# Kernel optimization log

Hardware: AMD Instinct MI355X
Metric: run time of the kernel (lower is better)

Reference implementation:

```python
import jax, jax.numpy as jnp
import numpy as np

N_LEVELS = 16
N_FEATURES = 2
RES_BASE = 16.0
RES_FINE = 512.0
LOG2_HASHMAP = 19
HASHMAP_SIZE = 1 << LOG2_HASHMAP
ROOM_MIN = np.zeros(3, np.float32)
ROOM_MAX = np.ones(3, np.float32)
# primes as uint32; low 19 bits of (corner * prime) match int64 math since
# low-k bits of a product depend only on low-k bits of the operands, and the
# final XOR is bitwise followed by mod 2**19 (a power of two -> bit mask).
PRIMES = np.array([1, 2654435761, 805459861], dtype=np.uint32)
# 8 trilinear corners in the same (dx,dy,dz) enumeration as the torch code
OFFSETS = np.array([[dx, dy, dz] for dx in (0, 1) for dy in (0, 1) for dz in (0, 1)], dtype=np.uint32)
OFFSETS_F = OFFSETS.astype(np.float32)


def setup_inputs() -> dict:
    key = jax.random.key(0)
    k1, k2 = jax.random.split(key)
    x = jax.random.uniform(k1, (1048576, 3), dtype=jnp.float32)  # points in unit cube
    embeddings = jax.random.uniform(k2, (HASHMAP_SIZE, N_FEATURES), dtype=jnp.float32,
                                    minval=-1e-4, maxval=1e-4)
    return {"x": x, "embeddings": embeddings}


def reference(x, embeddings):
    # growth factor b = exp((log(res_fine) - log(res_base)) / (L - 1))
    b = jnp.exp((jnp.log(jnp.float32(RES_FINE)) - jnp.log(jnp.float32(RES_BASE))) / (N_LEVELS - 1))
    x_norm = (x - ROOM_MIN) / (ROOM_MAX - ROOM_MIN)  # [N,3]
    feats = []
    for i in range(N_LEVELS):  # fixed small loop over levels
        res = jnp.floor(RES_BASE * b ** i)
        xs = x_norm * res                      # [N,3]
        xi = jnp.floor(xs)                     # [N,3]
        w = xs - xi                            # [N,3] trilinear weights
        corner = xi.astype(jnp.uint32)[:, None, :] + OFFSETS[None]  # [N,8,3]
        h = ((corner[..., 0] * PRIMES[0]) ^ (corner[..., 1] * PRIMES[1])
             ^ (corner[..., 2] * PRIMES[2])) & jnp.uint32(HASHMAP_SIZE - 1)  # [N,8]
        emb = embeddings[h]                    # [N,8,F] gather
        # corner weight = prod_d (off ? w : 1-w)
        cw = jnp.prod(OFFSETS_F[None] * w[:, None, :] + (1.0 - OFFSETS_F[None]) * (1.0 - w[:, None, :]), axis=-1)  # [N,8]
        feats.append(jnp.einsum('nc,ncf->nf', cw, emb))  # [N,F]
    return jnp.concatenate(feats, axis=-1)  # [N, L*F]
```

## Files before the change

### kernel.cpp

```cpp
#include <hip/hip_runtime.h>


#define TBL   (1u << 19)
#define MASK  (TBL - 1u)
#define P2    2654435761u
#define P3    805459861u
#define NBIN  4096
#define CAP   512
#define OVFCAP 65536

typedef _Float16 f16;
typedef f16 f16x2 __attribute__((ext_vector_type(2)));
typedef unsigned long long u64;

static __device__ __constant__ float c_res[16] = {
    16.f, 20.f, 25.f, 32.f, 40.f, 50.f, 64.f, 80.f,
    101.f, 128.f, 161.f, 203.f, 256.f, 322.f, 406.f, 512.f
};

__global__ __launch_bounds__(256) void k_prep(
    const float2* __restrict__ emb, f16x2* __restrict__ tbl,
    unsigned* __restrict__ cnt)
{
    int i = blockIdx.x * 256 + threadIdx.x;
    float2 v = emb[i];
    f16x2 h; h.x = (f16)v.x; h.y = (f16)v.y;
    tbl[i] = h;
    if (i <= NBIN) cnt[i] = 0u;
}

__global__ __launch_bounds__(256) void k_scatter(
    const float* __restrict__ x, unsigned* __restrict__ cnt,
    u64* __restrict__ rec, unsigned* __restrict__ ovf, int np)
{
    int p = blockIdx.x * 256 + threadIdx.x;
    if (p >= np) return;
    float px = x[3 * p + 0], py = x[3 * p + 1], pz = x[3 * p + 2];
    int cx = min(15, (int)(px * 16.0f));
    int cy = min(15, (int)(py * 16.0f));
    int cz = min(15, (int)(pz * 16.0f));
    unsigned key = (unsigned)((cx << 8) | (cy << 4) | cz);
    float fx = px * 16.0f - (float)cx;
    float fy = py * 16.0f - (float)cy;
    float fz = pz * 16.0f - (float)cz;
    unsigned qx = min(32767u, (unsigned)(fmaxf(fx, 0.0f) * 32768.0f));
    unsigned qy = min(32767u, (unsigned)(fmaxf(fy, 0.0f) * 32768.0f));
    unsigned qz = min(16383u, (unsigned)(fmaxf(fz, 0.0f) * 16384.0f));
    u64 r = ((u64)qx << 49) | ((u64)qy << 34) | ((u64)qz << 20) | (unsigned)p;

    unsigned slot = atomicAdd(&cnt[key], 1u);
    if (slot < CAP) {
        rec[(size_t)key * CAP + slot] = r;
    } else {
        unsigned o = atomicAdd(&cnt[NBIN], 1u);
        if (o < OVFCAP) ovf[o] = (unsigned)p;
    }
}

__device__ __forceinline__ void level_global(
    int l, float px, float py, float pz, const f16x2* __restrict__ t,
    float* o0, float* o1)
{
    float res = c_res[l];
    float sx = px * res, sy = py * res, sz = pz * res;
    float fx = floorf(sx), fy = floorf(sy), fz = floorf(sz);
    float wx1 = sx - fx, wy1 = sy - fy, wz1 = sz - fz;
    float wx0 = 1.0f - wx1, wy0 = 1.0f - wy1, wz0 = 1.0f - wz1;

    unsigned ux = (unsigned)fx, uy = (unsigned)fy, uz = (unsigned)fz;
    unsigned hx0 = ux, hx1 = ux + 1u;
    unsigned hy0 = uy * P2, hy1 = (uy + 1u) * P2;
    unsigned hz0 = uz * P3, hz1 = (uz + 1u) * P3;

    f16x2 e000 = t[(hx0 ^ hy0 ^ hz0) & MASK];
    f16x2 e001 = t[(hx0 ^ hy0 ^ hz1) & MASK];
    f16x2 e010 = t[(hx0 ^ hy1 ^ hz0) & MASK];
    f16x2 e011 = t[(hx0 ^ hy1 ^ hz1) & MASK];
    f16x2 e100 = t[(hx1 ^ hy0 ^ hz0) & MASK];
    f16x2 e101 = t[(hx1 ^ hy0 ^ hz1) & MASK];
    f16x2 e110 = t[(hx1 ^ hy1 ^ hz0) & MASK];
    f16x2 e111 = t[(hx1 ^ hy1 ^ hz1) & MASK];

    float wxy00 = wx0 * wy0, wxy01 = wx0 * wy1;
    float wxy10 = wx1 * wy0, wxy11 = wx1 * wy1;
    float c000 = wxy00 * wz0, c001 = wxy00 * wz1;
    float c010 = wxy01 * wz0, c011 = wxy01 * wz1;
    float c100 = wxy10 * wz0, c101 = wxy10 * wz1;
    float c110 = wxy11 * wz0, c111 = wxy11 * wz1;

    float f0 = c000 * (float)e000.x;
    float f1 = c000 * (float)e000.y;
    f0 = fmaf(c001, (float)e001.x, f0);  f1 = fmaf(c001, (float)e001.y, f1);
    f0 = fmaf(c010, (float)e010.x, f0);  f1 = fmaf(c010, (float)e010.y, f1);
    f0 = fmaf(c011, (float)e011.x, f0);  f1 = fmaf(c011, (float)e011.y, f1);
    f0 = fmaf(c100, (float)e100.x, f0);  f1 = fmaf(c100, (float)e100.y, f1);
    f0 = fmaf(c101, (float)e101.x, f0);  f1 = fmaf(c101, (float)e101.y, f1);
    f0 = fmaf(c110, (float)e110.x, f0);  f1 = fmaf(c110, (float)e110.y, f1);
    f0 = fmaf(c111, (float)e111.x, f0);  f1 = fmaf(c111, (float)e111.y, f1);
    *o0 = f0; *o1 = f1;
}

__device__ __forceinline__ unsigned fine_key(u64 r) {
    return ((((unsigned)(r >> 61)) & 7u) << 6) |
           ((((unsigned)(r >> 46)) & 7u) << 3) |
            (((unsigned)(r >> 31)) & 7u);
}

__global__ __launch_bounds__(256) void k_main(
    const u64* __restrict__ rec, const unsigned* __restrict__ cnt,
    const unsigned* __restrict__ ovf,
    const float* __restrict__ x, const f16x2* __restrict__ tbl,
    float* __restrict__ out, int np)
{
    int b = (int)(((blockIdx.x & 7u) << 9) | (blockIdx.x >> 3));
    int tid = threadIdx.x;
    float fbx = (float)(b >> 8), fby = (float)((b >> 4) & 15), fbz = (float)(b & 15);

    __shared__ u64 srec[CAP];
    __shared__ u64 ssort[CAP];
    __shared__ unsigned hist[512];
    __shared__ unsigned scn[256];
    __shared__ float sbuf[256 * 8];

    int n = min((int)cnt[b], CAP);

    for (int i = tid; i < n; i += 256) srec[i] = rec[(size_t)b * CAP + i];
    hist[tid] = 0u; hist[tid + 256] = 0u;
    __syncthreads();
    for (int i = tid; i < n; i += 256) atomicAdd(&hist[fine_key(srec[i])], 1u);
    __syncthreads();
    unsigned a0 = hist[2 * tid], a1 = hist[2 * tid + 1];
    unsigned s = a0 + a1;
    scn[tid] = s;
    __syncthreads();
    for (int d = 1; d < 256; d <<= 1) {
        unsigned v = (tid >= d) ? scn[tid - d] : 0u;
        __syncthreads();
        scn[tid] += v;
        __syncthreads();
    }
    unsigned excl = scn[tid] - s;
    hist[2 * tid] = excl;
    hist[2 * tid + 1] = excl + a0;
    __syncthreads();
    for (int i = tid; i < n; i += 256) {
        u64 r = srec[i];
        unsigned pos = atomicAdd(&hist[fine_key(r)], 1u);
        ssort[pos] = r;
    }
    __syncthreads();

    for (int i0 = 0; i0 < n; i0 += 256) {
        int nb = min(256, n - i0);
        bool act = tid < nb;
        u64 r = ssort[i0 + (act ? tid : 0)];
        unsigned qx = ((unsigned)(r >> 49)) & 32767u;
        unsigned qy = ((unsigned)(r >> 34)) & 32767u;
        unsigned qz = ((unsigned)(r >> 20)) & 16383u;
        float px = (fbx + ((float)qx + 0.5f) * (1.0f / 32768.0f)) * 0.0625f;
        float py = (fby + ((float)qy + 0.5f) * (1.0f / 32768.0f)) * 0.0625f;
        float pz = (fbz + ((float)qz + 0.5f) * (1.0f / 16384.0f)) * 0.0625f;

        #pragma unroll
        for (int g = 0; g < 4; ++g) {
            float fo[8];
            #pragma unroll
            for (int sl = 0; sl < 4; ++sl)
                level_global(4 * g + sl, px, py, pz, tbl, &fo[2 * sl], &fo[2 * sl + 1]);
            *(float4*)&sbuf[tid * 8 + 0] = *(float4*)&fo[0];
            *(float4*)&sbuf[tid * 8 + 4] = *(float4*)&fo[4];
            __syncthreads();
            for (int j = tid; j < 2 * nb; j += 256) {
                int pt = j >> 1, h = j & 1;
                unsigned pj = (unsigned)(ssort[i0 + pt] & 0xFFFFFu);
                float4 v = *(float4*)&sbuf[pt * 8 + h * 4];
                *(float4*)(out + (size_t)pj * 32 + g * 8 + h * 4) = v;
            }
            __syncthreads();
        }
    }

    unsigned oc = min(cnt[NBIN], (unsigned)OVFCAP);
    for (unsigned t = blockIdx.x * 256u + (unsigned)tid; t < oc; t += NBIN * 256u) {
        unsigned p = ovf[t];
        float px = x[3 * p + 0], py = x[3 * p + 1], pz = x[3 * p + 2];
        float* op = out + (size_t)p * 32;
        #pragma unroll
        for (int g = 0; g < 4; ++g) {
            float fo[8];
            #pragma unroll
            for (int sl = 0; sl < 4; ++sl)
                level_global(4 * g + sl, px, py, pz, tbl, &fo[2 * sl], &fo[2 * sl + 1]);
            ((float4*)op)[2 * g + 0] = *(float4*)&fo[0];
            ((float4*)op)[2 * g + 1] = *(float4*)&fo[4];
        }
    }
}

__global__ __launch_bounds__(256) void hashgrid_fwd(
    const float* __restrict__ x, const float* __restrict__ emb,
    float* __restrict__ out, int npts)
{
    int tid = blockIdx.x * 256 + threadIdx.x;
    int p = tid >> 4;
    int l = tid & 15;
    if (p >= npts) return;
    float px = x[p * 3], py = x[p * 3 + 1], pz = x[p * 3 + 2];
    float res = c_res[l];
    float sx = px * res, sy = py * res, sz = pz * res;
    float fx = floorf(sx), fy = floorf(sy), fz = floorf(sz);
    float wx1 = sx - fx, wy1 = sy - fy, wz1 = sz - fz;
    float wx0 = 1.0f - wx1, wy0 = 1.0f - wy1, wz0 = 1.0f - wz1;
    unsigned ux = (unsigned)fx, uy = (unsigned)fy, uz = (unsigned)fz;
    unsigned hx0 = ux, hx1 = ux + 1u;
    unsigned hy0 = uy * P2, hy1 = (uy + 1u) * P2;
    unsigned hz0 = uz * P3, hz1 = (uz + 1u) * P3;
    const float2* e = (const float2*)emb;
    float2 e000 = e[(hx0 ^ hy0 ^ hz0) & MASK];
    float2 e001 = e[(hx0 ^ hy0 ^ hz1) & MASK];
    float2 e010 = e[(hx0 ^ hy1 ^ hz0) & MASK];
    float2 e011 = e[(hx0 ^ hy1 ^ hz1) & MASK];
    float2 e100 = e[(hx1 ^ hy0 ^ hz0) & MASK];
    float2 e101 = e[(hx1 ^ hy0 ^ hz1) & MASK];
    float2 e110 = e[(hx1 ^ hy1 ^ hz0) & MASK];
    float2 e111 = e[(hx1 ^ hy1 ^ hz1) & MASK];
    float wxy00 = wx0 * wy0, wxy01 = wx0 * wy1;
    float wxy10 = wx1 * wy0, wxy11 = wx1 * wy1;
    float c000 = wxy00 * wz0, c001 = wxy00 * wz1;
    float c010 = wxy01 * wz0, c011 = wxy01 * wz1;
    float c100 = wxy10 * wz0, c101 = wxy10 * wz1;
    float c110 = wxy11 * wz0, c111 = wxy11 * wz1;
    float f0 = c000 * e000.x;
    float f1 = c000 * e000.y;
    f0 = fmaf(c001, e001.x, f0);  f1 = fmaf(c001, e001.y, f1);
    f0 = fmaf(c010, e010.x, f0);  f1 = fmaf(c010, e010.y, f1);
    f0 = fmaf(c011, e011.x, f0);  f1 = fmaf(c011, e011.y, f1);
    f0 = fmaf(c100, e100.x, f0);  f1 = fmaf(c100, e100.y, f1);
    f0 = fmaf(c101, e101.x, f0);  f1 = fmaf(c101, e101.y, f1);
    f0 = fmaf(c110, e110.x, f0);  f1 = fmaf(c110, e110.y, f1);
    f0 = fmaf(c111, e111.x, f0);  f1 = fmaf(c111, e111.y, f1);
    float2 o; o.x = f0; o.y = f1;
    ((float2*)out)[p * 16 + l] = o;
}

extern "C" void kernel_launch(void* const* d_in, const int* in_sizes, int n_in,
                              void* d_out, int out_size, void* d_ws, size_t ws_size,
                              hipStream_t stream) {
    const float* x   = (const float*)d_in[0];
    const float* emb = (const float*)d_in[1];
    float* out = (float*)d_out;
    int np = in_sizes[0] / 3;

    size_t szrec = (size_t)NBIN * CAP * 8;
    size_t sztbl = (size_t)TBL * 4;
    size_t szovf = (size_t)OVFCAP * 4;
    size_t szcnt = (size_t)(NBIN + 16) * 4;
    size_t need = szrec + sztbl + szovf + szcnt;

    if (ws_size >= need) {
        char* w = (char*)d_ws;
        u64*      rec = (u64*)(w);
        f16x2*    tbl = (f16x2*)(w + szrec);
        unsigned* ovf = (unsigned*)(w + szrec + sztbl);
        unsigned* cnt = (unsigned*)(w + szrec + sztbl + szovf);

        int pb = (np + 255) / 256;
        k_prep   <<<TBL / 256, 256, 0, stream>>>((const float2*)emb, tbl, cnt);
        k_scatter<<<pb, 256, 0, stream>>>(x, cnt, rec, ovf, np);
        k_main   <<<NBIN, 256, 0, stream>>>(rec, cnt, ovf, x, tbl, out, np);
    } else {
        int total = np * 16;
        hashgrid_fwd<<<(total + 255) / 256, 256, 0, stream>>>(x, emb, out, np);
    }
}
```

Before: 410.1 us.

## Split levels across threads: eight threads per point, two levels each

The main loop now assigns each point to eight threads, each computing two hash-grid levels and writing a 16-byte chunk of the output row directly with a nontemporal store. The shared-memory staging buffer and the per-group barriers used to coalesce output writes are removed. This raises parallelism per block and drops the barriers and LDS traffic. In exchange, coordinate decode is repeated eight times per point and the sorted-record read is duplicated.

Result: slower. 470.5 us (+14.7%).

```diff
diff --git a/kernel.cpp b/kernel.cpp
--- a/kernel.cpp
+++ b/kernel.cpp
@@ -11,11 +11,16 @@
 
 typedef _Float16 f16;
 typedef f16 f16x2 __attribute__((ext_vector_type(2)));
+typedef float f32x4 __attribute__((ext_vector_type(4)));
 typedef unsigned long long u64;
 
 static __device__ __constant__ float c_res[16] = {
     16.f, 20.f, 25.f, 32.f, 40.f, 50.f, 64.f, 80.f,
     101.f, 128.f, 161.f, 203.f, 256.f, 322.f, 406.f, 512.f
+};
+static __device__ __constant__ float2 c_res2[8] = {
+    {16.f, 20.f}, {25.f, 32.f}, {40.f, 50.f}, {64.f, 80.f},
+    {101.f, 128.f}, {161.f, 203.f}, {256.f, 322.f}, {406.f, 512.f}
 };
 
 __global__ __launch_bounds__(256) void k_prep(
@@ -57,11 +62,10 @@
     }
 }
 
-__device__ __forceinline__ void level_global(
-    int l, float px, float py, float pz, const f16x2* __restrict__ t,
+__device__ __forceinline__ void level_res(
+    float res, float px, float py, float pz, const f16x2* __restrict__ t,
     float* o0, float* o1)
 {
-    float res = c_res[l];
     float sx = px * res, sy = py * res, sz = pz * res;
     float fx = floorf(sx), fy = floorf(sy), fz = floorf(sz);
     float wx1 = sx - fx, wy1 = sy - fy, wz1 = sz - fz;
@@ -120,7 +124,6 @@
     __shared__ u64 ssort[CAP];
     __shared__ unsigned hist[512];
     __shared__ unsigned scn[256];
-    __shared__ float sbuf[256 * 8];
 
     int n = min((int)cnt[b], CAP);
 
@@ -150,33 +153,29 @@
     }
     __syncthreads();
 
-    for (int i0 = 0; i0 < n; i0 += 256) {
-        int nb = min(256, n - i0);
-        bool act = tid < nb;
-        u64 r = ssort[i0 + (act ? tid : 0)];
+    int nslot = n * 8;
+    for (int s0 = 0; s0 < nslot; s0 += 256) {
+        int sl = s0 + tid;
+        bool act = sl < nslot;
+        int pi = sl >> 3;
+        int ls = sl & 7;
+        u64 r = ssort[act ? pi : 0];
         unsigned qx = ((unsigned)(r >> 49)) & 32767u;
         unsigned qy = ((unsigned)(r >> 34)) & 32767u;
         unsigned qz = ((unsigned)(r >> 20)) & 16383u;
+        unsigned pj = (unsigned)(r & 0xFFFFFu);
         float px = (fbx + ((float)qx + 0.5f) * (1.0f / 32768.0f)) * 0.0625f;
         float py = (fby + ((float)qy + 0.5f) * (1.0f / 32768.0f)) * 0.0625f;
         float pz = (fbz + ((float)qz + 0.5f) * (1.0f / 16384.0f)) * 0.0625f;
 
-        #pragma unroll
-        for (int g = 0; g < 4; ++g) {
-            float fo[8];
-            #pragma unroll
-            for (int sl = 0; sl < 4; ++sl)
-                level_global(4 * g + sl, px, py, pz, tbl, &fo[2 * sl], &fo[2 * sl + 1]);
-            *(float4*)&sbuf[tid * 8 + 0] = *(float4*)&fo[0];
-            *(float4*)&sbuf[tid * 8 + 4] = *(float4*)&fo[4];
-            __syncthreads();
-            for (int j = tid; j < 2 * nb; j += 256) {
-                int pt = j >> 1, h = j & 1;
-                unsigned pj = (unsigned)(ssort[i0 + pt] & 0xFFFFFu);
-                float4 v = *(float4*)&sbuf[pt * 8 + h * 4];
-                *(float4*)(out + (size_t)pj * 32 + g * 8 + h * 4) = v;
-            }
-            __syncthreads();
+        float2 rr = c_res2[ls];
+        float fo0, fo1, fo2, fo3;
+        level_res(rr.x, px, py, pz, tbl, &fo0, &fo1);
+        level_res(rr.y, px, py, pz, tbl, &fo2, &fo3);
+
+        if (act) {
+            f32x4 v; v.x = fo0; v.y = fo1; v.z = fo2; v.w = fo3;
+            __builtin_nontemporal_store(v, (f32x4*)(out + (size_t)pj * 32 + ls * 4));
         }
     }
 
@@ -186,13 +185,12 @@
         float px = x[3 * p + 0], py = x[3 * p + 1], pz = x[3 * p + 2];
         float* op = out + (size_t)p * 32;
         #pragma unroll
-        for (int g = 0; g < 4; ++g) {
-            float fo[8];
-            #pragma unroll
-            for (int sl = 0; sl < 4; ++sl)
-                level_global(4 * g + sl, px, py, pz, tbl, &fo[2 * sl], &fo[2 * sl + 1]);
-            ((float4*)op)[2 * g + 0] = *(float4*)&fo[0];
-            ((float4*)op)[2 * g + 1] = *(float4*)&fo[4];
+        for (int g = 0; g < 8; ++g) {
+            float fo0, fo1, fo2, fo3;
+            level_res(c_res[2 * g], px, py, pz, tbl, &fo0, &fo1);
+            level_res(c_res[2 * g + 1], px, py, pz, tbl, &fo2, &fo3);
+            f32x4 v; v.x = fo0; v.y = fo1; v.z = fo2; v.w = fo3;
+            *(f32x4*)(op + g * 4) = v;
         }
     }
 }
```
